# Kernel optimization log

Measured on AMD Instinct MI355X. Metric: run time of the kernel, lower is better.

The kernel has to match this reference:

```python
import jax, jax.numpy as jnp
import numpy as np

N = 100000
E = 1000000
D_IN = 64
H1, C1 = 12, 12   # conv1: heads=12, out=12 -> concat 144
H2, C2 = 1, 64    # conv2: heads=1, out=64
NEG_SLOPE = 0.2
ALPHA = 0.5       # SSGConv alpha, K=1


def setup_inputs() -> dict:
    key = jax.random.key(0)
    ks = jax.random.split(key, 16)
    features = jax.random.normal(ks[0], (N, D_IN), dtype=jnp.float32)
    # edges with no self loops (PyG GATv2 removes then re-adds self loops)
    src = jax.random.randint(ks[1], (E,), 0, N)
    off = jax.random.randint(ks[2], (E,), 1, N)
    dst = (src + off) % N
    edge_index = jnp.stack([src, dst]).astype(jnp.int64)
    g = lambda k, shape, fan: (jax.random.normal(k, shape, jnp.float32) * (1.0 / np.sqrt(fan)))
    params = dict(
        W_ssg=g(ks[3], (D_IN, D_IN), D_IN), b_ssg=jnp.zeros((D_IN,), jnp.float32),
        W1l=g(ks[4], (D_IN, H1 * C1), D_IN), b1l=jnp.zeros((H1 * C1,), jnp.float32),
        W1r=g(ks[5], (D_IN, H1 * C1), D_IN), b1r=jnp.zeros((H1 * C1,), jnp.float32),
        att1=g(ks[6], (H1, C1), C1), bias1=jnp.zeros((H1 * C1,), jnp.float32),
        W2l=g(ks[7], (H1 * C1, H2 * C2), H1 * C1), b2l=jnp.zeros((H2 * C2,), jnp.float32),
        W2r=g(ks[8], (H1 * C1, H2 * C2), H1 * C1), b2r=jnp.zeros((H2 * C2,), jnp.float32),
        att2=g(ks[9], (H2, C2), C2), bias2=jnp.zeros((H2 * C2,), jnp.float32),
    )
    return dict(features=features, edge_index=edge_index, **params)


def _add_self_loops(src, dst):
    loop = jnp.arange(N, dtype=src.dtype)
    return jnp.concatenate([src, loop]), jnp.concatenate([dst, loop])


def _ssg_conv(x, src, dst, W, b):
    # gcn_norm with self loops, edge weight 1
    s, d = _add_self_loops(src, dst)
    deg = jax.ops.segment_sum(jnp.ones_like(s, dtype=x.dtype), d, num_segments=N)
    dinv = jnp.where(deg > 0, jax.lax.rsqrt(deg), 0.0)
    norm = dinv[s] * dinv[d]                      # [E+N]
    agg = jax.ops.segment_sum(x[s] * norm[:, None], d, num_segments=N)
    h = ALPHA * x + (1.0 - ALPHA) * agg           # K=1
    return h @ W + b


def _gatv2_conv(x, src, dst, Wl, bl, Wr, br, att, bias, Hh, Cc):
    s, d = _add_self_loops(src, dst)
    xl = (x @ Wl + bl).reshape(N, Hh, Cc)
    xr = (x @ Wr + br).reshape(N, Hh, Cc)
    e = jax.nn.leaky_relu(xl[s] + xr[d], NEG_SLOPE)       # [E', H, C]
    logits = jnp.einsum('ehc,hc->eh', e, att)             # [E', H]
    m = jax.ops.segment_max(logits, d, num_segments=N)    # [N, H]
    a = jnp.exp(logits - m[d])
    denom = jax.ops.segment_sum(a, d, num_segments=N)
    a = a / (denom[d] + 1e-16)                            # segment softmax
    out = jax.ops.segment_sum(xl[s] * a[:, :, None], d, num_segments=N)
    return out.reshape(N, Hh * Cc) + bias


def reference(features, edge_index, W_ssg, b_ssg, W1l, b1l, W1r, b1r,
              att1, bias1, W2l, b2l, W2r, b2r, att2, bias2):
    src, dst = edge_index[0], edge_index[1]
    x = _ssg_conv(features, src, dst, W_ssg, b_ssg)
    x = _gatv2_conv(x, src, dst, W1l, b1l, W1r, b1r, att1, bias1, H1, C1)
    x = _gatv2_conv(x, src, dst, W2l, b2l, W2r, b2r, att2, bias2, H2, C2)
    return x
```

## Files before the change

### kernel.cpp

```cpp
#include <hip/hip_runtime.h>

#define NNODE 100000
#define NEDGE 1000000
#define CAP 64

__device__ __forceinline__ float lrelu(float x){ return x >= 0.f ? x : 0.2f*x; }

__global__ void detect_kernel(const int* __restrict__ ei, int* __restrict__ flag){
    if (threadIdx.x == 0 && blockIdx.x == 0){
        int nz = 0;
        for (int i = 1; i < 64; i += 2) nz |= ei[i];
        flag[0] = (nz == 0) ? 1 : 0;
    }
}

__global__ __launch_bounds__(256) void scatter_kernel(const int* __restrict__ ei,
                                                      const int* __restrict__ flag,
                                                      int* __restrict__ cnt,
                                                      int* __restrict__ col){
    int e = blockIdx.x * 256 + threadIdx.x;
    if (e >= NEDGE) return;
    int s, d;
    if (flag[0]){ s = ei[2*e]; d = ei[2*(NEDGE + e)]; }
    else        { s = ei[e];   d = ei[NEDGE + e]; }
    if ((unsigned)s < NNODE && (unsigned)d < NNODE){
        int p = atomicAdd(&cnt[d], 1);
        if (p < CAP) col[d*CAP + p] = s;
    }
}

__global__ __launch_bounds__(256) void dinv_kernel(const int* __restrict__ cnt,
                                                   float* __restrict__ dinv){
    int i = blockIdx.x * 256 + threadIdx.x;
    if (i < NNODE) dinv[i] = rsqrtf((float)(cnt[i] + 1));
}

__global__ __launch_bounds__(256) void foldw_kernel(const float* __restrict__ Wssg,
                                                    const float* __restrict__ bssg,
                                                    const float* __restrict__ W1l,
                                                    const float* __restrict__ b1l,
                                                    const float* __restrict__ W1r,
                                                    const float* __restrict__ b1r,
                                                    float* __restrict__ Wcl,
                                                    float* __restrict__ Wcr,
                                                    float* __restrict__ bcl,
                                                    float* __restrict__ bcr){
    int id = blockIdx.x * 256 + threadIdx.x;
    if (id < 2*64*144){
        int which = id / (64*144);
        int rem = id - which*64*144;
        int k = rem / 144, j = rem - (rem/144)*144;
        const float* W1 = which ? W1r : W1l;
        float s = 0.f;
        #pragma unroll 8
        for (int c = 0; c < 64; ++c)
            s = fmaf(Wssg[k*64 + c], W1[c*144 + j], s);
        (which ? Wcr : Wcl)[k*144 + j] = s;
    }
    if (id < 2*144){
        int which = id / 144, j = id - which*144;
        const float* W1 = which ? W1r : W1l;
        const float* b1 = which ? b1r : b1l;
        float s = b1[j];
        #pragma unroll 8
        for (int c = 0; c < 64; ++c)
            s = fmaf(bssg[c], W1[c*144 + j], s);
        (which ? bcr : bcl)[j] = s;
    }
}

__global__ __launch_bounds__(256) void ssg_kernel(const float* __restrict__ x,
                                                  const int* __restrict__ col,
                                                  const int* __restrict__ cnt,
                                                  const float* __restrict__ dinv,
                                                  float* __restrict__ h){
    int wid = threadIdx.x >> 6, lane = threadIdx.x & 63;
    int d = blockIdx.x * 4 + wid;
    float di = dinv[d];
    float xd = x[(size_t)d*64 + lane];
    int deg = min(cnt[d], CAP);
    int myc = (lane < deg) ? col[d*CAP + lane] : 0;
    float wl  = (lane < deg) ? dinv[myc] : 0.f;
    float acc = 0.f;
    int s0 = __shfl(myc, 0);
    float w  = __shfl(wl, 0);
    float xv = (deg > 0) ? x[(size_t)s0*64 + lane] : 0.f;
    for (int k = 0; k < deg; ++k){
        int kn = (k+1 < deg) ? k+1 : 0;
        int s2 = __shfl(myc, kn);
        float w2 = __shfl(wl, kn);
        float xn = (k+1 < deg) ? x[(size_t)s2*64 + lane] : 0.f;
        acc = fmaf(xv, w, acc);
        xv = xn; w = w2;
    }
    float agg = fmaf(xd, di*di, di*acc);
    h[(size_t)d*64 + lane] = 0.5f*xd + 0.5f*agg;
}

template<int K, int OUT1, int OUT2>
__global__ __launch_bounds__(256, 4) void gemm2_kernel(const float* __restrict__ X,
                                                       const float* __restrict__ W1,
                                                       const float* __restrict__ B1,
                                                       const float* __restrict__ W2,
                                                       const float* __restrict__ B2,
                                                       float* __restrict__ Y1,
                                                       float* __restrict__ Y2){
    constexpr int OUT = OUT1 + OUT2;
    __shared__ float Xs[16][132];
    __shared__ float Ws[16][64];
    int row0 = blockIdx.x * 128, col0 = blockIdx.y * 64;
    int tid = threadIdx.x;
    int tc = tid & 15, tr = tid >> 4;
    int c0 = tc * 4, r0 = tr * 8;
    int srr = tid >> 2;
    int skk = (tid & 3) * 4;
    int swb = tid >> 6, swc = tid & 63;
    float acc[8][4] = {};
    for (int k0 = 0; k0 < K; k0 += 16){
        #pragma unroll
        for (int p = 0; p < 2; ++p){
            int r = srr + 64*p;
            int gr = row0 + r;
            float4 v = make_float4(0.f,0.f,0.f,0.f);
            if (gr < NNODE) v = *(const float4*)&X[(size_t)gr*K + k0 + skk];
            Xs[skk][r] = v.x; Xs[skk+1][r] = v.y; Xs[skk+2][r] = v.z; Xs[skk+3][r] = v.w;
        }
        #pragma unroll
        for (int p = 0; p < 4; ++p){
            int bb = swb + 4*p;
            int gc = col0 + swc;
            float wv = 0.f;
            if (gc < OUT)
                wv = (gc < OUT1) ? W1[(size_t)(k0+bb)*OUT1 + gc]
                                 : W2[(size_t)(k0+bb)*OUT2 + (gc-OUT1)];
            Ws[bb][swc] = wv;
        }
        __syncthreads();
        #pragma unroll
        for (int b = 0; b < 16; ++b){
            float4 xa = *(const float4*)&Xs[b][r0];
            float4 xb = *(const float4*)&Xs[b][r0+4];
            float4 w4 = *(const float4*)&Ws[b][c0];
            acc[0][0] = fmaf(xa.x, w4.x, acc[0][0]);
            acc[0][1] = fmaf(xa.x, w4.y, acc[0][1]);
            acc[0][2] = fmaf(xa.x, w4.z, acc[0][2]);
            acc[0][3] = fmaf(xa.x, w4.w, acc[0][3]);
            acc[1][0] = fmaf(xa.y, w4.x, acc[1][0]);
            acc[1][1] = fmaf(xa.y, w4.y, acc[1][1]);
            acc[1][2] = fmaf(xa.y, w4.z, acc[1][2]);
            acc[1][3] = fmaf(xa.y, w4.w, acc[1][3]);
            acc[2][0] = fmaf(xa.z, w4.x, acc[2][0]);
            acc[2][1] = fmaf(xa.z, w4.y, acc[2][1]);
            acc[2][2] = fmaf(xa.z, w4.z, acc[2][2]);
            acc[2][3] = fmaf(xa.z, w4.w, acc[2][3]);
            acc[3][0] = fmaf(xa.w, w4.x, acc[3][0]);
            acc[3][1] = fmaf(xa.w, w4.y, acc[3][1]);
            acc[3][2] = fmaf(xa.w, w4.z, acc[3][2]);
            acc[3][3] = fmaf(xa.w, w4.w, acc[3][3]);
            acc[4][0] = fmaf(xb.x, w4.x, acc[4][0]);
            acc[4][1] = fmaf(xb.x, w4.y, acc[4][1]);
            acc[4][2] = fmaf(xb.x, w4.z, acc[4][2]);
            acc[4][3] = fmaf(xb.x, w4.w, acc[4][3]);
            acc[5][0] = fmaf(xb.y, w4.x, acc[5][0]);
            acc[5][1] = fmaf(xb.y, w4.y, acc[5][1]);
            acc[5][2] = fmaf(xb.y, w4.z, acc[5][2]);
            acc[5][3] = fmaf(xb.y, w4.w, acc[5][3]);
            acc[6][0] = fmaf(xb.z, w4.x, acc[6][0]);
            acc[6][1] = fmaf(xb.z, w4.y, acc[6][1]);
            acc[6][2] = fmaf(xb.z, w4.z, acc[6][2]);
            acc[6][3] = fmaf(xb.z, w4.w, acc[6][3]);
            acc[7][0] = fmaf(xb.w, w4.x, acc[7][0]);
            acc[7][1] = fmaf(xb.w, w4.y, acc[7][1]);
            acc[7][2] = fmaf(xb.w, w4.z, acc[7][2]);
            acc[7][3] = fmaf(xb.w, w4.w, acc[7][3]);
        }
        __syncthreads();
    }
    #pragma unroll
    for (int i = 0; i < 8; ++i){
        int gr = row0 + r0 + i;
        if (gr >= NNODE) continue;
        #pragma unroll
        for (int j = 0; j < 4; ++j){
            int gc = col0 + c0 + j;
            if (gc < OUT){
                if (gc < OUT1) Y1[(size_t)gr*OUT1 + gc] = acc[i][j] + B1[gc];
                else           Y2[(size_t)gr*OUT2 + (gc - OUT1)] = acc[i][j] + B2[gc - OUT1];
            }
        }
    }
}

__global__ __launch_bounds__(192) void gat1_kernel(const float* __restrict__ xl,
                                                   float* __restrict__ xr,
                                                   const int* __restrict__ col,
                                                   const int* __restrict__ cnt,
                                                   const float* __restrict__ att,
                                                   const float* __restrict__ bias){
    __shared__ __align__(16) float V[16][148];
    __shared__ float A[16][13];
    __shared__ float lpart[12][4];
    __shared__ int scol[65];
    int d = blockIdx.x, t = threadIdx.x;
    int deg = min(cnt[d], CAP);
    int ne = deg + 1;
    if (t < deg) scol[t] = col[d*CAP + t];
    if (t == deg) scol[t] = d;
    int h = t % 12;
    int eslot = t / 12;
    float xrr[12], attr[12];
    #pragma unroll
    for (int c = 0; c < 12; ++c){
        xrr[c]  = xr[(size_t)d*144 + h*12 + c];
        attr[c] = att[h*12 + c];
    }
    int hh = t / 12;
    int u = t - 144, lh_h = u >> 2, lh_q = u & 3;
    float acc = 0.f, lacc = 0.f;
    __syncthreads();
    for (int e0 = 0; e0 < ne; e0 += 16){
        int e = e0 + eslot;
        if (e < ne){
            const float* row = &xl[(size_t)scol[e]*144 + h*12];
            float4 r0 = *(const float4*)(row);
            float4 r1 = *(const float4*)(row + 4);
            float4 r2 = *(const float4*)(row + 8);
            float s = 0.f;
            s = fmaf(lrelu(r0.x + xrr[0]),  attr[0],  s);
            s = fmaf(lrelu(r0.y + xrr[1]),  attr[1],  s);
            s = fmaf(lrelu(r0.z + xrr[2]),  attr[2],  s);
            s = fmaf(lrelu(r0.w + xrr[3]),  attr[3],  s);
            s = fmaf(lrelu(r1.x + xrr[4]),  attr[4],  s);
            s = fmaf(lrelu(r1.y + xrr[5]),  attr[5],  s);
            s = fmaf(lrelu(r1.z + xrr[6]),  attr[6],  s);
            s = fmaf(lrelu(r1.w + xrr[7]),  attr[7],  s);
            s = fmaf(lrelu(r2.x + xrr[8]),  attr[8],  s);
            s = fmaf(lrelu(r2.y + xrr[9]),  attr[9],  s);
            s = fmaf(lrelu(r2.z + xrr[10]), attr[10], s);
            s = fmaf(lrelu(r2.w + xrr[11]), attr[11], s);
            A[eslot][h] = __expf(s);
            *(float4*)&V[eslot][h*12]     = r0;
            *(float4*)&V[eslot][h*12 + 4] = r1;
            *(float4*)&V[eslot][h*12 + 8] = r2;
        }
        __syncthreads();
        int lim = ne - e0; if (lim > 16) lim = 16;
        if (t < 144){
            for (int ee = 0; ee < lim; ++ee)
                acc = fmaf(A[ee][hh], V[ee][t], acc);
        } else {
            #pragma unroll
            for (int i = 0; i < 4; ++i){
                int ee = lh_q*4 + i;
                if (ee < lim) lacc += A[ee][lh_h];
            }
        }
        __syncthreads();
    }
    if (t >= 144) lpart[lh_h][lh_q] = lacc;
    __syncthreads();
    if (t < 144){
        float l = lpart[hh][0] + lpart[hh][1] + lpart[hh][2] + lpart[hh][3];
        xr[(size_t)d*144 + t] = acc / (l + 1e-16f) + bias[t];
    }
}

__global__ __launch_bounds__(256) void gat2_kernel(const float* __restrict__ xl,
                                                   const float* __restrict__ xr,
                                                   const int* __restrict__ col,
                                                   const int* __restrict__ cnt,
                                                   const float* __restrict__ att,
                                                   const float* __restrict__ bias,
                                                   float* __restrict__ out){
    __shared__ float V[4][8][68];
    __shared__ float Aw[4][8];
    int wid = threadIdx.x >> 6, lane = threadIdx.x & 63;
    int d0 = blockIdx.x * 4;
    int d = d0 + wid;
    int deg = min(cnt[d], 63);
    int ne = deg + 1;
    int nemax = 1;
    #pragma unroll
    for (int j = 0; j < 4; ++j) nemax = max(nemax, min(cnt[d0+j], 63) + 1);
    int eq = lane >> 3, cq = lane & 7;
    float4 xra = *(const float4*)&xr[(size_t)d*64 + 8*cq];
    float4 xrb = *(const float4*)&xr[(size_t)d*64 + 8*cq + 4];
    float4 ata = *(const float4*)&att[8*cq];
    float4 atb = *(const float4*)&att[8*cq + 4];
    int myc = (lane < deg) ? col[d*CAP + lane] : d;
    float acc = 0.f, l = 0.f;
    for (int e0 = 0; e0 < nemax; e0 += 8){
        int e = e0 + eq;
        bool val = (e < ne);
        int se = __shfl(myc, val ? e : 0);
        float4 va = make_float4(0.f,0.f,0.f,0.f), vb = va;
        if (val){
            va = *(const float4*)&xl[(size_t)se*64 + 8*cq];
            vb = *(const float4*)&xl[(size_t)se*64 + 8*cq + 4];
        }
        float part = 0.f;
        part = fmaf(lrelu(va.x + xra.x), ata.x, part);
        part = fmaf(lrelu(va.y + xra.y), ata.y, part);
        part = fmaf(lrelu(va.z + xra.z), ata.z, part);
        part = fmaf(lrelu(va.w + xra.w), ata.w, part);
        part = fmaf(lrelu(vb.x + xrb.x), atb.x, part);
        part = fmaf(lrelu(vb.y + xrb.y), atb.y, part);
        part = fmaf(lrelu(vb.z + xrb.z), atb.z, part);
        part = fmaf(lrelu(vb.w + xrb.w), atb.w, part);
        part += __shfl_xor(part, 1);
        part += __shfl_xor(part, 2);
        part += __shfl_xor(part, 4);
        *(float4*)&V[wid][eq][8*cq]     = va;
        *(float4*)&V[wid][eq][8*cq + 4] = vb;
        if (cq == 0) Aw[wid][eq] = val ? __expf(part) : 0.f;
        __syncthreads();
        int lim = ne - e0; if (lim > 8) lim = 8;
        for (int j = 0; j < lim; ++j){
            float a = Aw[wid][j];
            l += a;
            acc = fmaf(a, V[wid][j][lane], acc);
        }
        __syncthreads();
    }
    out[(size_t)d*64 + lane] = acc / (l + 1e-16f) + bias[lane];
}

extern "C" void kernel_launch(void* const* d_in, const int* in_sizes, int n_in,
                              void* d_out, int out_size, void* d_ws, size_t ws_size,
                              hipStream_t stream){
    const float* feat  = (const float*)d_in[0];
    const int*   ei    = (const int*)d_in[1];
    const float* W_ssg = (const float*)d_in[2];
    const float* b_ssg = (const float*)d_in[3];
    const float* W1l   = (const float*)d_in[4];
    const float* b1l   = (const float*)d_in[5];
    const float* W1r   = (const float*)d_in[6];
    const float* b1r   = (const float*)d_in[7];
    const float* att1  = (const float*)d_in[8];
    const float* bias1 = (const float*)d_in[9];
    const float* W2l   = (const float*)d_in[10];
    const float* b2l   = (const float*)d_in[11];
    const float* W2r   = (const float*)d_in[12];
    const float* b2r   = (const float*)d_in[13];
    const float* att2  = (const float*)d_in[14];
    const float* bias2 = (const float*)d_in[15];
    float* out = (float*)d_out;

    char* ws = (char*)d_ws;
    size_t off = 0;
    auto alloc = [&](size_t bytes)->void*{
        void* p = ws + off; off = (off + bytes + 255) & ~(size_t)255; return p;
    };
    int*   flag = (int*)  alloc(4);
    int*   cnt  = (int*)  alloc((size_t)NNODE*4);
    int*   col  = (int*)  alloc((size_t)NNODE*CAP*4);
    float* dinv = (float*)alloc((size_t)NNODE*4);
    float* h    = (float*)alloc((size_t)NNODE*64*4);
    float* x1   = (float*)alloc((size_t)NNODE*64*4);
    float* xl1  = (float*)alloc((size_t)NNODE*144*4);
    float* xr1  = (float*)alloc((size_t)NNODE*144*4);
    float* Wcl  = (float*)alloc((size_t)64*144*4);
    float* Wcr  = (float*)alloc((size_t)64*144*4);
    float* bcl  = (float*)alloc((size_t)144*4);
    float* bcr  = (float*)alloc((size_t)144*4);
    float* xl2  = h;
    float* xr2  = x1;

    hipMemsetAsync(cnt, 0, (size_t)NNODE*4, stream);
    detect_kernel<<<1, 64, 0, stream>>>(ei, flag);
    scatter_kernel<<<(NEDGE + 255)/256, 256, 0, stream>>>(ei, flag, cnt, col);
    dinv_kernel<<<(NNODE + 255)/256, 256, 0, stream>>>(cnt, dinv);
    foldw_kernel<<<72, 256, 0, stream>>>(W_ssg, b_ssg, W1l, b1l, W1r, b1r,
                                         Wcl, Wcr, bcl, bcr);

    ssg_kernel<<<NNODE/4, 256, 0, stream>>>(feat, col, cnt, dinv, h);

    gemm2_kernel<64,144,144><<<dim3(782,5), 256, 0, stream>>>(
        h, Wcl, bcl, Wcr, bcr, xl1, xr1);

    gat1_kernel<<<NNODE, 192, 0, stream>>>(xl1, xr1, col, cnt, att1, bias1);

    gemm2_kernel<144,64,64><<<dim3(782,2), 256, 0, stream>>>(
        xr1, W2l, b2l, W2r, b2r, xl2, xr2);

    gat2_kernel<<<NNODE/4, 256, 0, stream>>>(xl2, xr2, col, cnt, att2, bias2, out);
}
```

Baseline: 593.3 us.

## Store intermediates in bf16 and run node GEMMs on MFMA bf16 instructions

Intermediate activations (SSG output, GAT projections, GAT1 output) are now stored as bf16, and both dense projections use a new MFMA 16x16x32 bf16 GEMM kernel that reads pre-transposed bf16 weights directly from global memory. The SSG aggregation is restructured so four edges are gathered in parallel with float4 loads and then reduced across lanes. GAT1 folds the softmax denominator into the main accumulation loop and drops the separate partial-sum threads. This halves the gather and stream traffic and moves GEMM work onto matrix cores, at the cost of bf16 rounding error in all intermediates.

```diff
diff --git a/kernel.cpp b/kernel.cpp
--- a/kernel.cpp
+++ b/kernel.cpp
@@ -4,7 +4,18 @@
 #define NEDGE 1000000
 #define CAP 64
 
+typedef __attribute__((ext_vector_type(4))) float f32x4;
+typedef __attribute__((ext_vector_type(8))) short bf16x8;
+
 __device__ __forceinline__ float lrelu(float x){ return x >= 0.f ? x : 0.2f*x; }
+__device__ __forceinline__ unsigned short f2bf(float f){
+    unsigned u = __float_as_uint(f);
+    unsigned r = (u + 0x7FFFu + ((u >> 16) & 1u)) >> 16;
+    return (unsigned short)r;
+}
+__device__ __forceinline__ float bf2f(unsigned short h){
+    return __uint_as_float(((unsigned)h) << 16);
+}
 
 __global__ void detect_kernel(const int* __restrict__ ei, int* __restrict__ flag){
     if (threadIdx.x == 0 && blockIdx.x == 0){
@@ -41,10 +52,8 @@
                                                     const float* __restrict__ b1l,
                                                     const float* __restrict__ W1r,
                                                     const float* __restrict__ b1r,
-                                                    float* __restrict__ Wcl,
-                                                    float* __restrict__ Wcr,
-                                                    float* __restrict__ bcl,
-                                                    float* __restrict__ bcr){
+                                                    unsigned short* __restrict__ Wct,
+                                                    float* __restrict__ bc){
     int id = blockIdx.x * 256 + threadIdx.x;
     if (id < 2*64*144){
         int which = id / (64*144);
@@ -55,7 +64,7 @@
         #pragma unroll 8
         for (int c = 0; c < 64; ++c)
             s = fmaf(Wssg[k*64 + c], W1[c*144 + j], s);
-        (which ? Wcr : Wcl)[k*144 + j] = s;
+        Wct[(size_t)(which*144 + j)*64 + k] = f2bf(s);
     }
     if (id < 2*144){
         int which = id / 144, j = id - which*144;
@@ -65,141 +74,121 @@
         #pragma unroll 8
         for (int c = 0; c < 64; ++c)
             s = fmaf(bssg[c], W1[c*144 + j], s);
-        (which ? bcr : bcl)[j] = s;
-    }
+        bc[which*144 + j] = s;
+    }
+}
+
+__global__ __launch_bounds__(256) void castw2_kernel(const float* __restrict__ W2l,
+                                                     const float* __restrict__ b2l,
+                                                     const float* __restrict__ W2r,
+                                                     const float* __restrict__ b2r,
+                                                     unsigned short* __restrict__ W2t,
+                                                     float* __restrict__ b2c){
+    int id = blockIdx.x * 256 + threadIdx.x;
+    if (id < 128*160){
+        int j = id / 160, k = id - (id/160)*160;
+        float v = 0.f;
+        if (k < 144) v = (j < 64) ? W2l[k*64 + j] : W2r[k*64 + (j - 64)];
+        W2t[(size_t)j*160 + k] = f2bf(v);
+    }
+    if (id < 128) b2c[id] = (id < 64) ? b2l[id] : b2r[id - 64];
 }
 
 __global__ __launch_bounds__(256) void ssg_kernel(const float* __restrict__ x,
                                                   const int* __restrict__ col,
                                                   const int* __restrict__ cnt,
                                                   const float* __restrict__ dinv,
-                                                  float* __restrict__ h){
+                                                  unsigned short* __restrict__ hb){
     int wid = threadIdx.x >> 6, lane = threadIdx.x & 63;
     int d = blockIdx.x * 4 + wid;
+    int cq = lane & 15, eq = lane >> 4;
     float di = dinv[d];
-    float xd = x[(size_t)d*64 + lane];
     int deg = min(cnt[d], CAP);
     int myc = (lane < deg) ? col[d*CAP + lane] : 0;
-    float wl  = (lane < deg) ? dinv[myc] : 0.f;
-    float acc = 0.f;
-    int s0 = __shfl(myc, 0);
-    float w  = __shfl(wl, 0);
-    float xv = (deg > 0) ? x[(size_t)s0*64 + lane] : 0.f;
-    for (int k = 0; k < deg; ++k){
-        int kn = (k+1 < deg) ? k+1 : 0;
-        int s2 = __shfl(myc, kn);
-        float w2 = __shfl(wl, kn);
-        float xn = (k+1 < deg) ? x[(size_t)s2*64 + lane] : 0.f;
-        acc = fmaf(xv, w, acc);
-        xv = xn; w = w2;
-    }
-    float agg = fmaf(xd, di*di, di*acc);
-    h[(size_t)d*64 + lane] = 0.5f*xd + 0.5f*agg;
+    float wl = (lane < deg) ? dinv[myc] : 0.f;
+    float a0 = 0.f, a1 = 0.f, a2 = 0.f, a3 = 0.f;
+    for (int e0 = 0; e0 < deg; e0 += 4){
+        int e = e0 + eq;
+        bool val = e < deg;
+        int idx = val ? e : 0;
+        int se = __shfl(myc, idx);
+        float w = __shfl(wl, idx);
+        if (!val) w = 0.f;
+        float4 v = *(const float4*)&x[(size_t)se*64 + 4*cq];
+        a0 = fmaf(w, v.x, a0);
+        a1 = fmaf(w, v.y, a1);
+        a2 = fmaf(w, v.z, a2);
+        a3 = fmaf(w, v.w, a3);
+    }
+    #pragma unroll
+    for (int m = 16; m < 64; m <<= 1){
+        a0 += __shfl_xor(a0, m);
+        a1 += __shfl_xor(a1, m);
+        a2 += __shfl_xor(a2, m);
+        a3 += __shfl_xor(a3, m);
+    }
+    if (eq == 0){
+        float4 xd = *(const float4*)&x[(size_t)d*64 + 4*cq];
+        float dd = di*di;
+        ushort4 o;
+        o.x = f2bf(0.5f*xd.x + 0.5f*fmaf(di, a0, dd*xd.x));
+        o.y = f2bf(0.5f*xd.y + 0.5f*fmaf(di, a1, dd*xd.y));
+        o.z = f2bf(0.5f*xd.z + 0.5f*fmaf(di, a2, dd*xd.z));
+        o.w = f2bf(0.5f*xd.w + 0.5f*fmaf(di, a3, dd*xd.w));
+        *(ushort4*)&hb[(size_t)d*64 + 4*cq] = o;
+    }
 }
 
 template<int K, int OUT1, int OUT2>
-__global__ __launch_bounds__(256, 4) void gemm2_kernel(const float* __restrict__ X,
-                                                       const float* __restrict__ W1,
-                                                       const float* __restrict__ B1,
-                                                       const float* __restrict__ W2,
-                                                       const float* __restrict__ B2,
-                                                       float* __restrict__ Y1,
-                                                       float* __restrict__ Y2){
+__global__ __launch_bounds__(256) void gemm_mfma_kernel(const unsigned short* __restrict__ Xb,
+                                                        const unsigned short* __restrict__ Wt,
+                                                        const float* __restrict__ Bc,
+                                                        unsigned short* __restrict__ Y1,
+                                                        unsigned short* __restrict__ Y2){
     constexpr int OUT = OUT1 + OUT2;
-    __shared__ float Xs[16][132];
-    __shared__ float Ws[16][64];
-    int row0 = blockIdx.x * 128, col0 = blockIdx.y * 64;
-    int tid = threadIdx.x;
-    int tc = tid & 15, tr = tid >> 4;
-    int c0 = tc * 4, r0 = tr * 8;
-    int srr = tid >> 2;
-    int skk = (tid & 3) * 4;
-    int swb = tid >> 6, swc = tid & 63;
-    float acc[8][4] = {};
-    for (int k0 = 0; k0 < K; k0 += 16){
+    constexpr int NT = OUT / 16;
+    int wid = threadIdx.x >> 6, lane = threadIdx.x & 63;
+    int m = lane & 15, kg = lane >> 4;
+    int row0 = blockIdx.x * 64 + wid * 16;
+    int rA = row0 + m; if (rA > NNODE-1) rA = NNODE-1;
+    f32x4 acc[NT];
+    #pragma unroll
+    for (int t = 0; t < NT; ++t) acc[t] = (f32x4){0.f, 0.f, 0.f, 0.f};
+    #pragma unroll
+    for (int k0 = 0; k0 < K; k0 += 32){
+        bf16x8 a = *(const bf16x8*)&Xb[(size_t)rA*K + k0 + 8*kg];
         #pragma unroll
-        for (int p = 0; p < 2; ++p){
-            int r = srr + 64*p;
-            int gr = row0 + r;
-            float4 v = make_float4(0.f,0.f,0.f,0.f);
-            if (gr < NNODE) v = *(const float4*)&X[(size_t)gr*K + k0 + skk];
-            Xs[skk][r] = v.x; Xs[skk+1][r] = v.y; Xs[skk+2][r] = v.z; Xs[skk+3][r] = v.w;
-        }
+        for (int t = 0; t < NT; ++t){
+            bf16x8 b = *(const bf16x8*)&Wt[(size_t)(t*16 + m)*K + k0 + 8*kg];
+            acc[t] = __builtin_amdgcn_mfma_f32_16x16x32_bf16(a, b, acc[t], 0, 0, 0);
+        }
+    }
+    int rbase = row0 + 4*kg;
+    #pragma unroll
+    for (int t = 0; t < NT; ++t){
+        int colg = t*16 + m;
+        float bias = Bc[colg];
         #pragma unroll
-        for (int p = 0; p < 4; ++p){
-            int bb = swb + 4*p;
-            int gc = col0 + swc;
-            float wv = 0.f;
-            if (gc < OUT)
-                wv = (gc < OUT1) ? W1[(size_t)(k0+bb)*OUT1 + gc]
-                                 : W2[(size_t)(k0+bb)*OUT2 + (gc-OUT1)];
-            Ws[bb][swc] = wv;
-        }
-        __syncthreads();
-        #pragma unroll
-        for (int b = 0; b < 16; ++b){
-            float4 xa = *(const float4*)&Xs[b][r0];
-            float4 xb = *(const float4*)&Xs[b][r0+4];
-            float4 w4 = *(const float4*)&Ws[b][c0];
-            acc[0][0] = fmaf(xa.x, w4.x, acc[0][0]);
-            acc[0][1] = fmaf(xa.x, w4.y, acc[0][1]);
-            acc[0][2] = fmaf(xa.x, w4.z, acc[0][2]);
-            acc[0][3] = fmaf(xa.x, w4.w, acc[0][3]);
-            acc[1][0] = fmaf(xa.y, w4.x, acc[1][0]);
-            acc[1][1] = fmaf(xa.y, w4.y, acc[1][1]);
-            acc[1][2] = fmaf(xa.y, w4.z, acc[1][2]);
-            acc[1][3] = fmaf(xa.y, w4.w, acc[1][3]);
-            acc[2][0] = fmaf(xa.z, w4.x, acc[2][0]);
-            acc[2][1] = fmaf(xa.z, w4.y, acc[2][1]);
-            acc[2][2] = fmaf(xa.z, w4.z, acc[2][2]);
-            acc[2][3] = fmaf(xa.z, w4.w, acc[2][3]);
-            acc[3][0] = fmaf(xa.w, w4.x, acc[3][0]);
-            acc[3][1] = fmaf(xa.w, w4.y, acc[3][1]);
-            acc[3][2] = fmaf(xa.w, w4.z, acc[3][2]);
-            acc[3][3] = fmaf(xa.w, w4.w, acc[3][3]);
-            acc[4][0] = fmaf(xb.x, w4.x, acc[4][0]);
-            acc[4][1] = fmaf(xb.x, w4.y, acc[4][1]);
-            acc[4][2] = fmaf(xb.x, w4.z, acc[4][2]);
-            acc[4][3] = fmaf(xb.x, w4.w, acc[4][3]);
-            acc[5][0] = fmaf(xb.y, w4.x, acc[5][0]);
-            acc[5][1] = fmaf(xb.y, w4.y, acc[5][1]);
-            acc[5][2] = fmaf(xb.y, w4.z, acc[5][2]);
-            acc[5][3] = fmaf(xb.y, w4.w, acc[5][3]);
-            acc[6][0] = fmaf(xb.z, w4.x, acc[6][0]);
-            acc[6][1] = fmaf(xb.z, w4.y, acc[6][1]);
-            acc[6][2] = fmaf(xb.z, w4.z, acc[6][2]);
-            acc[6][3] = fmaf(xb.z, w4.w, acc[6][3]);
-            acc[7][0] = fmaf(xb.w, w4.x, acc[7][0]);
-            acc[7][1] = fmaf(xb.w, w4.y, acc[7][1]);
-            acc[7][2] = fmaf(xb.w, w4.z, acc[7][2]);
-            acc[7][3] = fmaf(xb.w, w4.w, acc[7][3]);
-        }
-        __syncthreads();
-    }
-    #pragma unroll
-    for (int i = 0; i < 8; ++i){
-        int gr = row0 + r0 + i;
-        if (gr >= NNODE) continue;
-        #pragma unroll
-        for (int j = 0; j < 4; ++j){
-            int gc = col0 + c0 + j;
-            if (gc < OUT){
-                if (gc < OUT1) Y1[(size_t)gr*OUT1 + gc] = acc[i][j] + B1[gc];
-                else           Y2[(size_t)gr*OUT2 + (gc - OUT1)] = acc[i][j] + B2[gc - OUT1];
+        for (int r = 0; r < 4; ++r){
+            int gr = rbase + r;
+            if (gr < NNODE){
+                unsigned short v = f2bf(acc[t][r] + bias);
+                if (colg < OUT1) Y1[(size_t)gr*OUT1 + colg] = v;
+                else             Y2[(size_t)gr*OUT2 + (colg - OUT1)] = v;
             }
         }
     }
 }
 
-__global__ __launch_bounds__(192) void gat1_kernel(const float* __restrict__ xl,
-                                                   float* __restrict__ xr,
+__global__ __launch_bounds__(192) void gat1_kernel(const unsigned short* __restrict__ xl,
+                                                   const unsigned short* __restrict__ xr,
                                                    const int* __restrict__ col,
                                                    const int* __restrict__ cnt,
                                                    const float* __restrict__ att,
-                                                   const float* __restrict__ bias){
+                                                   const float* __restrict__ bias,
+                                                   unsigned short* __restrict__ xg){
     __shared__ __align__(16) float V[16][148];
     __shared__ float A[16][13];
-    __shared__ float lpart[12][4];
     __shared__ int scol[65];
     int d = blockIdx.x, t = threadIdx.x;
     int deg = min(cnt[d], CAP);
@@ -209,64 +198,65 @@
     int h = t % 12;
     int eslot = t / 12;
     float xrr[12], attr[12];
-    #pragma unroll
-    for (int c = 0; c < 12; ++c){
-        xrr[c]  = xr[(size_t)d*144 + h*12 + c];
-        attr[c] = att[h*12 + c];
-    }
+    {
+        const ushort4* xrp = (const ushort4*)&xr[(size_t)d*144 + h*12];
+        ushort4 q0 = xrp[0], q1 = xrp[1], q2 = xrp[2];
+        xrr[0]=bf2f(q0.x); xrr[1]=bf2f(q0.y); xrr[2]=bf2f(q0.z); xrr[3]=bf2f(q0.w);
+        xrr[4]=bf2f(q1.x); xrr[5]=bf2f(q1.y); xrr[6]=bf2f(q1.z); xrr[7]=bf2f(q1.w);
+        xrr[8]=bf2f(q2.x); xrr[9]=bf2f(q2.y); xrr[10]=bf2f(q2.z); xrr[11]=bf2f(q2.w);
+    }
+    #pragma unroll
+    for (int c = 0; c < 12; ++c) attr[c] = att[h*12 + c];
     int hh = t / 12;
-    int u = t - 144, lh_h = u >> 2, lh_q = u & 3;
-    float acc = 0.f, lacc = 0.f;
+    float acc = 0.f, l = 0.f;
     __syncthreads();
     for (int e0 = 0; e0 < ne; e0 += 16){
         int e = e0 + eslot;
         if (e < ne){
-            const float* row = &xl[(size_t)scol[e]*144 + h*12];
-            float4 r0 = *(const float4*)(row);
-            float4 r1 = *(const float4*)(row + 4);
-            float4 r2 = *(const float4*)(row + 8);
+            const ushort4* row = (const ushort4*)&xl[(size_t)scol[e]*144 + h*12];
+            ushort4 q0 = row[0], q1 = row[1], q2 = row[2];
+            float v0=bf2f(q0.x), v1=bf2f(q0.y), v2=bf2f(q0.z), v3=bf2f(q0.w);
+            float v4=bf2f(q1.x), v5=bf2f(q1.y), v6=bf2f(q1.z), v7=bf2f(q1.w);
+            float v8=bf2f(q2.x), v9=bf2f(q2.y), v10=bf2f(q2.z), v11=bf2f(q2.w);
             float s = 0.f;
-            s = fmaf(lrelu(r0.x + xrr[0]),  attr[0],  s);
-            s = fmaf(lrelu(r0.y + xrr[1]),  attr[1],  s);
-            s = fmaf(lrelu(r0.z + xrr[2]),  attr[2],  s);
-            s = fmaf(lrelu(r0.w + xrr[3]),  attr[3],  s);
-            s = fmaf(lrelu(r1.x + xrr[4]),  attr[4],  s);
-            s = fmaf(lrelu(r1.y + xrr[5]),  attr[5],  s);
-            s = fmaf(lrelu(r1.z + xrr[6]),  attr[6],  s);
-            s = fmaf(lrelu(r1.w + xrr[7]),  attr[7],  s);
-            s = fmaf(lrelu(r2.x + xrr[8]),  attr[8],  s);
-            s = fmaf(lrelu(r2.y + xrr[9]),  attr[9],  s);
-            s = fmaf(lrelu(r2.z + xrr[10]), attr[10], s);
-            s = fmaf(lrelu(r2.w + xrr[11]), attr[11], s);
+            s = fmaf(lrelu(v0 + xrr[0]),  attr[0],  s);
+            s = fmaf(lrelu(v1 + xrr[1]),  attr[1],  s);
+            s = fmaf(lrelu(v2 + xrr[2]),  attr[2],  s);
+            s = fmaf(lrelu(v3 + xrr[3]),  attr[3],  s);
+            s = fmaf(lrelu(v4 + xrr[4]),  attr[4],  s);
+            s = fmaf(lrelu(v5 + xrr[5]),  attr[5],  s);
+            s = fmaf(lrelu(v6 + xrr[6]),  attr[6],  s);
+            s = fmaf(lrelu(v7 + xrr[7]),  attr[7],  s);
+            s = fmaf(lrelu(v8 + xrr[8]),  attr[8],  s);
+            s = fmaf(lrelu(v9 + xrr[9]),  attr[9],  s);
+            s = fmaf(lrelu(v10 + xrr[10]), attr[10], s);
+            s = fmaf(lrelu(v11 + xrr[11]), attr[11], s);
             A[eslot][h] = __expf(s);
-            *(float4*)&V[eslot][h*12]     = r0;
-            *(float4*)&V[eslot][h*12 + 4] = r1;
-            *(float4*)&V[eslot][h*12 + 8] = r2;
+            float4 f0 = make_float4(v0, v1, v2, v3);
+            float4 f1 = make_float4(v4, v5, v6, v7);
+            float4 f2 = make_float4(v8, v9, v10, v11);
+            *(float4*)&V[eslot][h*12]     = f0;
+            *(float4*)&V[eslot][h*12 + 4] = f1;
+            *(float4*)&V[eslot][h*12 + 8] = f2;
         }
         __syncthreads();
-        int lim = ne - e0; if (lim > 16) lim = 16;
         if (t < 144){
-            for (int ee = 0; ee < lim; ++ee)
-                acc = fmaf(A[ee][hh], V[ee][t], acc);
-        } else {
-            #pragma unroll
-            for (int i = 0; i < 4; ++i){
-                int ee = lh_q*4 + i;
-                if (ee < lim) lacc += A[ee][lh_h];
+            int lim = ne - e0; if (lim > 16) lim = 16;
+            for (int ee = 0; ee < lim; ++ee){
+                float a  = A[ee][hh];
+                float xv = V[ee][t];
+                l += a;
+                acc = fmaf(a, xv, acc);
             }
         }
         __syncthreads();
     }
-    if (t >= 144) lpart[lh_h][lh_q] = lacc;
-    __syncthreads();
-    if (t < 144){
-        float l = lpart[hh][0] + lpart[hh][1] + lpart[hh][2] + lpart[hh][3];
-        xr[(size_t)d*144 + t] = acc / (l + 1e-16f) + bias[t];
-    }
-}
-
-__global__ __launch_bounds__(256) void gat2_kernel(const float* __restrict__ xl,
-                                                   const float* __restrict__ xr,
+    if (t < 144) xg[(size_t)d*160 + t] = f2bf(acc / (l + 1e-16f) + bias[t]);
+    else if (t < 160) xg[(size_t)d*160 + t] = 0;
+}
+
+__global__ __launch_bounds__(256) void gat2_kernel(const unsigned short* __restrict__ xl,
+                                                   const unsigned short* __restrict__ xr,
                                                    const int* __restrict__ col,
                                                    const int* __restrict__ cnt,
                                                    const float* __restrict__ att,
@@ -283,8 +273,13 @@
     #pragma unroll
     for (int j = 0; j < 4; ++j) nemax = max(nemax, min(cnt[d0+j], 63) + 1);
     int eq = lane >> 3, cq = lane & 7;
-    float4 xra = *(const float4*)&xr[(size_t)d*64 + 8*cq];
-    float4 xrb = *(const float4*)&xr[(size_t)d*64 + 8*cq + 4];
+    float4 xra, xrb;
+    {
+        ushort4 u0 = *(const ushort4*)&xr[(size_t)d*64 + 8*cq];
+        ushort4 u1 = *(const ushort4*)&xr[(size_t)d*64 + 8*cq + 4];
+        xra = make_float4(bf2f(u0.x), bf2f(u0.y), bf2f(u0.z), bf2f(u0.w));
+        xrb = make_float4(bf2f(u1.x), bf2f(u1.y), bf2f(u1.z), bf2f(u1.w));
+    }
     float4 ata = *(const float4*)&att[8*cq];
     float4 atb = *(const float4*)&att[8*cq + 4];
     int myc = (lane < deg) ? col[d*CAP + lane] : d;
@@ -295,8 +290,10 @@
         int se = __shfl(myc, val ? e : 0);
         float4 va = make_float4(0.f,0.f,0.f,0.f), vb = va;
         if (val){
-            va = *(const float4*)&xl[(size_t)se*64 + 8*cq];
-            vb = *(const float4*)&xl[(size_t)se*64 + 8*cq + 4];
+            ushort4 u0 = *(const ushort4*)&xl[(size_t)se*64 + 8*cq];
+            ushort4 u1 = *(const ushort4*)&xl[(size_t)se*64 + 8*cq + 4];
+            va = make_float4(bf2f(u0.x), bf2f(u0.y), bf2f(u0.z), bf2f(u0.w));
+            vb = make_float4(bf2f(u1.x), bf2f(u1.y), bf2f(u1.z), bf2f(u1.w));
         }
         float part = 0.f;
         part = fmaf(lrelu(va.x + xra.x), ata.x, part);
@@ -351,37 +348,35 @@
     auto alloc = [&](size_t bytes)->void*{
         void* p = ws + off; off = (off + bytes + 255) & ~(size_t)255; return p;
     };
-    int*   flag = (int*)  alloc(4);
-    int*   cnt  = (int*)  alloc((size_t)NNODE*4);
-    int*   col  = (int*)  alloc((size_t)NNODE*CAP*4);
-    float* dinv = (float*)alloc((size_t)NNODE*4);
-    float* h    = (float*)alloc((size_t)NNODE*64*4);
-    float* x1   = (float*)alloc((size_t)NNODE*64*4);
-    float* xl1  = (float*)alloc((size_t)NNODE*144*4);
-    float* xr1  = (float*)alloc((size_t)NNODE*144*4);
-    float* Wcl  = (float*)alloc((size_t)64*144*4);
-    float* Wcr  = (float*)alloc((size_t)64*144*4);
-    float* bcl  = (float*)alloc((size_t)144*4);
-    float* bcr  = (float*)alloc((size_t)144*4);
-    float* xl2  = h;
-    float* xr2  = x1;
+    int*            flag = (int*)           alloc(4);
+    int*            cnt  = (int*)           alloc((size_t)NNODE*4);
+    int*            col  = (int*)           alloc((size_t)NNODE*CAP*4);
+    float*          dinv = (float*)         alloc((size_t)NNODE*4);
+    unsigned short* hb   = (unsigned short*)alloc((size_t)NNODE*64*2);
+    unsigned short* xl1b = (unsigned short*)alloc((size_t)NNODE*144*2);
+    unsigned short* xr1b = (unsigned short*)alloc((size_t)NNODE*144*2);
+    unsigned short* xg   = (unsigned short*)alloc((size_t)NNODE*160*2);
+    unsigned short* xl2b = (unsigned short*)alloc((size_t)NNODE*64*2);
+    unsigned short* xr2b = (unsigned short*)alloc((size_t)NNODE*64*2);
+    unsigned short* Wct  = (unsigned short*)alloc((size_t)288*64*2);
+    float*          bc   = (float*)         alloc((size_t)288*4);
+    unsigned short* W2t  = (unsigned short*)alloc((size_t)128*160*2);
+    float*          b2c  = (float*)         alloc((size_t)128*4);
 
     hipMemsetAsync(cnt, 0, (size_t)NNODE*4, stream);
     detect_kernel<<<1, 64, 0, stream>>>(ei, flag);
     scatter_kernel<<<(NEDGE + 255)/256, 256, 0, stream>>>(ei, flag, cnt, col);
     dinv_kernel<<<(NNODE + 255)/256, 256, 0, stream>>>(cnt, dinv);
-    foldw_kernel<<<72, 256, 0, stream>>>(W_ssg, b_ssg, W1l, b1l, W1r, b1r,
-                                         Wcl, Wcr, bcl, bcr);
-
-    ssg_kernel<<<NNODE/4, 256, 0, stream>>>(feat, col, cnt, dinv, h);
-
-    gemm2_kernel<64,144,144><<<dim3(782,5), 256, 0, stream>>>(
-        h, Wcl, bcl, Wcr, bcr, xl1, xr1);
-
-    gat1_kernel<<<NNODE, 192, 0, stream>>>(xl1, xr1, col, cnt, att1, bias1);
-
-    gemm2_kernel<144,64,64><<<dim3(782,2), 256, 0, stream>>>(
-        xr1, W2l, b2l, W2r, b2r, xl2, xr2);
-
-    gat2_kernel<<<NNODE/4, 256, 0, stream>>>(xl2, xr2, col, cnt, att2, bias2, out);
-}
+    foldw_kernel<<<72, 256, 0, stream>>>(W_ssg, b_ssg, W1l, b1l, W1r, b1r, Wct, bc);
+    castw2_kernel<<<80, 256, 0, stream>>>(W2l, b2l, W2r, b2r, W2t, b2c);
+
+    ssg_kernel<<<NNODE/4, 256, 0, stream>>>(feat, col, cnt, dinv, hb);
+
+    gemm_mfma_kernel<64,144,144><<<1563, 256, 0, stream>>>(hb, Wct, bc, xl1b, xr1b);
+
+    gat1_kernel<<<NNODE, 192, 0, stream>>>(xl1b, xr1b, col, cnt, att1, bias1, xg);
+
+    gemm_mfma_kernel<160,64,64><<<1563, 256, 0, stream>>>(xg, W2t, b2c, xl2b, xr2b);
+
+    gat2_kernel<<<NNODE/4, 256, 0, stream>>>(xl2b, xr2b, col, cnt, att2, bias2, out);
+}
```

Result: faster. 493.5 us (-16.8%).
